# Performance work log

Measured on AMD Instinct MI355X. Metric: run time of the kernel, lower is better.

## Reference

```python
import jax, jax.numpy as jnp
import numpy as np

N_NODES = 100000


def _add_self_loops(edge_index, n):
    loop = jnp.arange(n, dtype=edge_index.dtype)
    src = jnp.concatenate([edge_index[0], loop])
    dst = jnp.concatenate([edge_index[1], loop])
    return src, dst


def _gcn_conv(x, W, b, src, dst, n):
    # h = X W, then symmetric-normalized scatter-add over edges (PyG GCNConv)
    h = x @ W
    ones = jnp.ones(src.shape[0], dtype=h.dtype)
    deg = jax.ops.segment_sum(ones, dst, num_segments=n)  # in-degree incl. self loops
    dinv = jnp.where(deg > 0, jax.lax.rsqrt(deg), 0.0)
    norm = dinv[src] * dinv[dst]                           # [E]
    msg = h[src] * norm[:, None]                           # gather + scale
    out = jax.ops.segment_sum(msg, dst, num_segments=n)    # scatter-add
    return out + b


def setup_inputs() -> dict:
    key = jax.random.key(0)
    k1, k2, k3, k4 = jax.random.split(key, 4)
    F, H, C = 128, 128, 16
    x = jax.random.normal(k1, (N_NODES, F), dtype=jnp.float32)
    edge_index = jax.random.randint(k2, (2, 1600000), 0, N_NODES, dtype=jnp.int64)
    W1 = jax.random.normal(k3, (F, H), dtype=jnp.float32) / np.sqrt(F)
    b1 = jnp.zeros((H,), dtype=jnp.float32)
    W2 = jax.random.normal(k4, (H, C), dtype=jnp.float32) / np.sqrt(H)
    b2 = jnp.zeros((C,), dtype=jnp.float32)
    return {"x": x, "edge_index": edge_index, "W1": W1, "b1": b1, "W2": W2, "b2": b2}


def reference(x, edge_index, W1, b1, W2, b2):
    n = x.shape[0]
    src, dst = _add_self_loops(edge_index, n)
    h = _gcn_conv(x, W1, b1, src, dst, n)
    h = jax.nn.relu(h)
    # dropout(p=0.1) treated as identity (deterministic eval-mode reference)
    logits = _gcn_conv(h, W2, b2, src, dst, n)
    return logits, jax.nn.log_softmax(logits, axis=1)
```

## Files before the change

### kernel.cpp

```cpp
#include <hip/hip_runtime.h>
#include <math.h>


#define ELLW 72
#define EPB 16384
#define BSH 9
#define MAXEB 100
#define MAXBK 200

typedef __attribute__((ext_vector_type(8))) short short8;
typedef __attribute__((ext_vector_type(4))) float f32x4;
typedef __attribute__((ext_vector_type(4))) int i32x4;
typedef __attribute__((ext_vector_type(4))) _Float16 f16x4;

__device__ __forceinline__ float bf2f(unsigned short u) {
    return __uint_as_float(((unsigned int)u) << 16);
}
__device__ __forceinline__ unsigned short f2bf(float f) {
    unsigned int u = __float_as_uint(f);
    unsigned int r = (u + 0x7fffu + ((u >> 16) & 1u)) >> 16;
    return (unsigned short)r;
}
__device__ __forceinline__ f32x4 h2f4(f16x4 v) {
    f32x4 r;
    r[0] = (float)v[0]; r[1] = (float)v[1]; r[2] = (float)v[2]; r[3] = (float)v[3];
    return r;
}

__global__ void k_prep_hist(unsigned short* __restrict__ h, _Float16* __restrict__ g,
                            const float* __restrict__ W1, unsigned short* __restrict__ wt,
                            int n, const int* __restrict__ dst, int E,
                            int* __restrict__ hist, int nbuck) {
    __shared__ int lh[MAXBK];
    const int t = threadIdx.x;
    if (blockIdx.x < 64) {
        int i = blockIdx.x * 256 + t;
        if (i < 16384) {
            int nc = i >> 7, k = i & 127;
            wt[i] = f2bf(W1[k * 128 + nc]);
        }
        if (i < 128) h[(size_t)n * 128 + i] = 0;
        if (i < 16) g[(size_t)n * 16 + i] = (_Float16)0.f;
        return;
    }
    const int blk = blockIdx.x - 64;
    for (int i = t; i < nbuck; i += 256) lh[i] = 0;
    __syncthreads();
    const int e0 = blk * EPB;
    const int e1 = min(e0 + EPB, E);
    for (int e = e0 + t; e < e1; e += 256)
        atomicAdd(&lh[dst[e] >> BSH], 1);
    __syncthreads();
    for (int i = t; i < nbuck; i += 256)
        hist[blk * nbuck + i] = lh[i];
}

__global__ void k_scan(int* __restrict__ hist, int* __restrict__ bstart,
                       int* __restrict__ bcount, int neb, int nbuck) {
    __shared__ unsigned short lh[MAXEB * MAXBK];
    __shared__ int sc[256];
    const int t = threadIdx.x;
    const int items = neb * nbuck;
    const int it4 = items >> 2;
    for (int i = t; i < it4; i += 256) {
        i32x4 v = *(const i32x4*)(hist + i * 4);
        lh[i * 4 + 0] = (unsigned short)v[0];
        lh[i * 4 + 1] = (unsigned short)v[1];
        lh[i * 4 + 2] = (unsigned short)v[2];
        lh[i * 4 + 3] = (unsigned short)v[3];
    }
    for (int i = (it4 << 2) + t; i < items; i += 256)
        lh[i] = (unsigned short)hist[i];
    __syncthreads();
    int total = 0;
    if (t < nbuck)
        for (int blk = 0; blk < neb; ++blk) total += lh[blk * nbuck + t];
    sc[t] = total;
    __syncthreads();
    for (int o = 1; o < 256; o <<= 1) {
        int x = 0;
        if (t >= o) x = sc[t - o];
        __syncthreads();
        if (t >= o) sc[t] += x;
        __syncthreads();
    }
    if (t < nbuck) {
        int run = sc[t] - total;
        bstart[t] = run;
        bcount[t] = total;
        for (int blk = 0; blk < neb; ++blk) {
            int idx = blk * nbuck + t;
            int v = lh[idx];
            hist[idx] = run;
            run += v;
        }
    }
}

__global__ void k_bin(const int* __restrict__ src, const int* __restrict__ dst, int E,
                      const int* __restrict__ hist, int* __restrict__ binned, int nbuck) {
    __shared__ int cnt[MAXBK];
    const int t = threadIdx.x, blk = blockIdx.x;
    for (int i = t; i < nbuck; i += 256) cnt[i] = hist[blk * nbuck + i];
    __syncthreads();
    const int e0 = blk * EPB;
    const int e1 = min(e0 + EPB, E);
    for (int e = e0 + t; e < e1; e += 256) {
        int d = dst[e];
        int b = d >> BSH;
        int pos = atomicAdd(&cnt[b], 1);
        binned[pos] = src[e] | ((d & ((1 << BSH) - 1)) << 17);
    }
}

__global__ void k_ell(const int* __restrict__ binned, const int* __restrict__ bstart,
                      const int* __restrict__ bcount, int* __restrict__ deg,
                      int* __restrict__ col, int n) {
    __shared__ int ldeg[1 << BSH];
    const int t = threadIdx.x, b = blockIdx.x;
    const int node0 = b << BSH;
    for (int i = t; i < (1 << BSH); i += 256) ldeg[i] = 0;
    __syncthreads();
    const int st = bstart[b], cv = bcount[b];
    for (int i = t; i < cv; i += 256) {
        int v = binned[st + i];
        int s = v & 0x1FFFF;
        int dl = v >> 17;
        int q = atomicAdd(&ldeg[dl], 1);
        if (q < ELLW) col[(size_t)(node0 + dl) * ELLW + q] = s;
    }
    __syncthreads();
    for (int i = t; i < (1 << BSH); i += 256) {
        int node = node0 + i;
        if (node < n) {
            int dgv = ldeg[i];
            deg[node] = dgv;
            int dc = dgv > ELLW ? ELLW : dgv;
            int kend = (dc + 7) & ~7;
            for (int q = dc; q < kend; ++q) col[(size_t)node * ELLW + q] = n;
        }
    }
}

__global__ void k_gemm1(const float* __restrict__ x, const unsigned short* __restrict__ wt,
                        const int* __restrict__ deg, unsigned short* __restrict__ h,
                        int n) {
    __shared__ unsigned short xs[64 * 136];
    const int t = threadIdx.x;
    const int row0 = blockIdx.x * 64;
    for (int i = t; i < 2048; i += 256) {
        int r = i >> 5, c4 = (i & 31) << 2;
        int gr = row0 + r;
        float4 v = make_float4(0.f, 0.f, 0.f, 0.f);
        if (gr < n) v = *(const float4*)(x + (size_t)gr * 128 + c4);
        ushort4 u;
        u.x = f2bf(v.x); u.y = f2bf(v.y); u.z = f2bf(v.z); u.w = f2bf(v.w);
        *(ushort4*)(xs + r * 136 + c4) = u;
    }
    __syncthreads();
    const int w = t >> 6;
    const int lane = t & 63;
    const int m = lane & 15, q = lane >> 4;
    f32x4 acc[8];
#pragma unroll
    for (int ns = 0; ns < 8; ++ns) acc[ns] = (f32x4){0.f, 0.f, 0.f, 0.f};
#pragma unroll
    for (int kt = 0; kt < 4; ++kt) {
        short8 a = *(const short8*)(xs + (w * 16 + m) * 136 + kt * 32 + q * 8);
#pragma unroll
        for (int ns = 0; ns < 8; ++ns) {
            short8 b = *(const short8*)((const short*)wt + (ns * 16 + m) * 128 + kt * 32 + q * 8);
            acc[ns] = __builtin_amdgcn_mfma_f32_16x16x32_bf16(a, b, acc[ns], 0, 0, 0);
        }
    }
    unsigned short* xsw = xs + (w * 16) * 136;
    float srow[4];
#pragma unroll
    for (int reg = 0; reg < 4; ++reg) {
        int gr = row0 + w * 16 + q * 4 + reg;
        srow[reg] = (gr < n) ? rsqrtf((float)(deg[gr] + 1)) : 0.f;
    }
#pragma unroll
    for (int ns = 0; ns < 8; ++ns)
#pragma unroll
        for (int reg = 0; reg < 4; ++reg)
            xsw[(q * 4 + reg) * 136 + ns * 16 + m] = f2bf(acc[ns][reg] * srow[reg]);
    __syncthreads();
#pragma unroll
    for (int it = 0; it < 8; ++it) {
        int rl = (lane >> 5) + it * 2;
        int off = (lane & 31) * 4;
        int gr = row0 + w * 16 + rl;
        if (gr < n)
            *(ushort4*)(h + (size_t)gr * 128 + off) = *(const ushort4*)(xsw + rl * 136 + off);
    }
}

__global__ __launch_bounds__(256, 2) void k_gather1f(
        const unsigned short* __restrict__ h, const int* __restrict__ deg,
        const int* __restrict__ col, const float* __restrict__ b1,
        const float* __restrict__ W2, _Float16* __restrict__ g, int n) {
    const int t = threadIdx.x;
    const int lane = t & 15;
    const int d = blockIdx.x * 16 + (t >> 4);
    if (d >= n) return;
    int dg = deg[d];
    if (dg > ELLW) dg = ELLW;
    const float dd = rsqrtf((float)(dg + 1));
    const int kend = (dg + 7) & ~7;
    const int* ecol = col + (size_t)d * ELLW;

    float aA[8], aB[8];
    {
        short8 u = *(const short8*)(h + (size_t)d * 128 + lane * 8);
#pragma unroll
        for (int j = 0; j < 8; ++j) {
            aA[j] = bf2f((unsigned short)u[j]);
            aB[j] = 0.f;
        }
    }
    for (int k = 0; k < kend; k += 8) {
        int4 c0 = *(const int4*)(ecol + k);
        int4 c1 = *(const int4*)(ecol + k + 4);
        short8 u0 = *(const short8*)(h + (size_t)c0.x * 128 + lane * 8);
        short8 u1 = *(const short8*)(h + (size_t)c0.y * 128 + lane * 8);
        short8 u2 = *(const short8*)(h + (size_t)c0.z * 128 + lane * 8);
        short8 u3 = *(const short8*)(h + (size_t)c0.w * 128 + lane * 8);
        short8 u4 = *(const short8*)(h + (size_t)c1.x * 128 + lane * 8);
        short8 u5 = *(const short8*)(h + (size_t)c1.y * 128 + lane * 8);
        short8 u6 = *(const short8*)(h + (size_t)c1.z * 128 + lane * 8);
        short8 u7 = *(const short8*)(h + (size_t)c1.w * 128 + lane * 8);
#pragma unroll
        for (int j = 0; j < 8; ++j) {
            aA[j] += bf2f((unsigned short)u0[j]) + bf2f((unsigned short)u2[j]) +
                     bf2f((unsigned short)u4[j]) + bf2f((unsigned short)u6[j]);
            aB[j] += bf2f((unsigned short)u1[j]) + bf2f((unsigned short)u3[j]) +
                     bf2f((unsigned short)u5[j]) + bf2f((unsigned short)u7[j]);
        }
    }
    float y[8];
    const float* b1p = b1 + lane * 8;
#pragma unroll
    for (int j = 0; j < 8; ++j)
        y[j] = fmaxf(fmaf(aA[j] + aB[j], dd, b1p[j]), 0.f);
    const float4* w2v = (const float4*)(W2 + lane * 8 * 16);
    float4 z0 = make_float4(0.f, 0.f, 0.f, 0.f);
    float4 z1 = z0, z2 = z0, z3 = z0;
#pragma unroll
    for (int j = 0; j < 8; ++j) {
        float4 w0 = w2v[j * 4 + 0], w1 = w2v[j * 4 + 1];
        float4 w2 = w2v[j * 4 + 2], w3 = w2v[j * 4 + 3];
        float yj = y[j];
        z0.x = fmaf(yj, w0.x, z0.x); z0.y = fmaf(yj, w0.y, z0.y);
        z0.z = fmaf(yj, w0.z, z0.z); z0.w = fmaf(yj, w0.w, z0.w);
        z1.x = fmaf(yj, w1.x, z1.x); z1.y = fmaf(yj, w1.y, z1.y);
        z1.z = fmaf(yj, w1.z, z1.z); z1.w = fmaf(yj, w1.w, z1.w);
        z2.x = fmaf(yj, w2.x, z2.x); z2.y = fmaf(yj, w2.y, z2.y);
        z2.z = fmaf(yj, w2.z, z2.z); z2.w = fmaf(yj, w2.w, z2.w);
        z3.x = fmaf(yj, w3.x, z3.x); z3.y = fmaf(yj, w3.y, z3.y);
        z3.z = fmaf(yj, w3.z, z3.z); z3.w = fmaf(yj, w3.w, z3.w);
    }
#pragma unroll
    for (int mm = 1; mm < 16; mm <<= 1) {
        z0.x += __shfl_xor(z0.x, mm); z0.y += __shfl_xor(z0.y, mm);
        z0.z += __shfl_xor(z0.z, mm); z0.w += __shfl_xor(z0.w, mm);
        z1.x += __shfl_xor(z1.x, mm); z1.y += __shfl_xor(z1.y, mm);
        z1.z += __shfl_xor(z1.z, mm); z1.w += __shfl_xor(z1.w, mm);
        z2.x += __shfl_xor(z2.x, mm); z2.y += __shfl_xor(z2.y, mm);
        z2.z += __shfl_xor(z2.z, mm); z2.w += __shfl_xor(z2.w, mm);
        z3.x += __shfl_xor(z3.x, mm); z3.y += __shfl_xor(z3.y, mm);
        z3.z += __shfl_xor(z3.z, mm); z3.w += __shfl_xor(z3.w, mm);
    }
    if (lane < 4) {
        float4 z = (lane == 0) ? z0 : (lane == 1) ? z1 : (lane == 2) ? z2 : z3;
        f16x4 zz;
        zz[0] = (_Float16)(z.x * dd); zz[1] = (_Float16)(z.y * dd);
        zz[2] = (_Float16)(z.z * dd); zz[3] = (_Float16)(z.w * dd);
        *(f16x4*)(g + (size_t)d * 16 + lane * 4) = zz;
    }
}

__global__ void k_gather2(const _Float16* __restrict__ g, const int* __restrict__ deg,
                          const int* __restrict__ col, const float* __restrict__ b2,
                          float* __restrict__ out, int n) {
    const int t = threadIdx.x;
    const int d = blockIdx.x * 64 + (t >> 2);
    if (d >= n) return;
    const int l = t & 3;
    int dg = deg[d];
    if (dg > ELLW) dg = ELLW;
    const float dd = rsqrtf((float)(dg + 1));
    const int kend = (dg + 7) & ~7;
    const int* ecol = col + (size_t)d * ELLW;
    const _Float16* gl = g + l * 4;

    f32x4 aA = h2f4(*(const f16x4*)(gl + (size_t)d * 16));
    f32x4 aB = (f32x4){0.f, 0.f, 0.f, 0.f};
    f32x4 aC = aB, aD = aB;
    for (int k = 0; k < kend; k += 8) {
        int4 c0 = *(const int4*)(ecol + k);
        int4 c1 = *(const int4*)(ecol + k + 4);
        f16x4 h0 = *(const f16x4*)(gl + (size_t)c0.x * 16);
        f16x4 h1 = *(const f16x4*)(gl + (size_t)c0.y * 16);
        f16x4 h2 = *(const f16x4*)(gl + (size_t)c0.z * 16);
        f16x4 h3 = *(const f16x4*)(gl + (size_t)c0.w * 16);
        f16x4 h4 = *(const f16x4*)(gl + (size_t)c1.x * 16);
        f16x4 h5 = *(const f16x4*)(gl + (size_t)c1.y * 16);
        f16x4 h6 = *(const f16x4*)(gl + (size_t)c1.z * 16);
        f16x4 h7 = *(const f16x4*)(gl + (size_t)c1.w * 16);
        aA += h2f4(h0); aB += h2f4(h1); aC += h2f4(h2); aD += h2f4(h3);
        aA += h2f4(h4); aB += h2f4(h5); aC += h2f4(h6); aD += h2f4(h7);
    }
    f32x4 bv = *(const f32x4*)(b2 + l * 4);
    f32x4 acc = (aA + aB + aC + aD) * dd + bv;
    *(f32x4*)(out + (size_t)d * 16 + l * 4) = acc;
    float m = fmaxf(fmaxf(acc[0], acc[1]), fmaxf(acc[2], acc[3]));
    m = fmaxf(m, __shfl_xor(m, 1));
    m = fmaxf(m, __shfl_xor(m, 2));
    float e = expf(acc[0] - m) + expf(acc[1] - m) + expf(acc[2] - m) + expf(acc[3] - m);
    e += __shfl_xor(e, 1);
    e += __shfl_xor(e, 2);
    float ls = m + logf(e);
    f32x4 o;
    o[0] = acc[0] - ls; o[1] = acc[1] - ls; o[2] = acc[2] - ls; o[3] = acc[3] - ls;
    *(f32x4*)(out + (size_t)n * 16 + (size_t)d * 16 + l * 4) = o;
}

static inline size_t align256(size_t v) { return (v + 255) & ~(size_t)255; }

extern "C" void kernel_launch(void* const* d_in, const int* in_sizes, int n_in,
                              void* d_out, int out_size, void* d_ws, size_t ws_size,
                              hipStream_t stream) {
    const float* x  = (const float*)d_in[0];
    const int*   ei = (const int*)d_in[1];
    const float* W1 = (const float*)d_in[2];
    const float* b1 = (const float*)d_in[3];
    const float* W2 = (const float*)d_in[4];
    const float* b2 = (const float*)d_in[5];
    float* out = (float*)d_out;

    const int n = in_sizes[0] / 128;
    const int E = in_sizes[1] / 2;
    const int* src = ei;
    const int* dst = ei + E;
    const int NEB = (E + EPB - 1) / EPB;
    const int NBUCK = (n + (1 << BSH) - 1) >> BSH;

    char* base = (char*)d_ws;
    size_t off = 0;
    int* deg = (int*)(base + off); off = align256(off + (size_t)n * 4);
    int* col = (int*)(base + off); off = align256(off + (size_t)n * ELLW * 4);
    unsigned short* wt = (unsigned short*)(base + off); off = align256(off + 128 * 128 * 2);
    unsigned short* h = (unsigned short*)(base + off); off = align256(off + ((size_t)n + 1) * 128 * 2);
    _Float16* g = (_Float16*)(base + off); off = align256(off + ((size_t)n + 1) * 16 * 2);
    int* hist = (int*)(base + off); off = align256(off + (size_t)MAXEB * MAXBK * 4);
    int* bstart = (int*)(base + off); off = align256(off + (size_t)MAXBK * 4);
    int* bcount = (int*)(base + off); off = align256(off + (size_t)MAXBK * 4);
    int* binned = (int*)(base + off); off = align256(off + (size_t)E * 4);

    k_prep_hist<<<64 + NEB, 256, 0, stream>>>(h, g, W1, wt, n, dst, E, hist, NBUCK);
    k_scan<<<1, 256, 0, stream>>>(hist, bstart, bcount, NEB, NBUCK);
    k_bin<<<NEB, 256, 0, stream>>>(src, dst, E, hist, binned, NBUCK);
    k_ell<<<NBUCK, 256, 0, stream>>>(binned, bstart, bcount, deg, col, n);

    k_gemm1<<<(n + 63) / 64, 256, 0, stream>>>(x, wt, deg, h, n);
    k_gather1f<<<(n + 15) / 16, 256, 0, stream>>>(h, deg, col, b1, W2, g, n);

    k_gather2<<<(n + 63) / 64, 256, 0, stream>>>(g, deg, col, b2, out, n);
}
```

Measured before the change: 351.4 us.

## Merge edge binning with GEMM1 and move degree normalization into gather

Binning blocks and GEMM1 blocks now run in one launch, so the dense XW1 product overlaps the edge binning and no longer has to wait for degrees. Because GEMM1 can run before degrees are known, the source-side scaling leaves the GEMM epilogue. A per-node dinv array is built in k_ell and applied per neighbour inside gather1f. This costs an extra 4-byte gather per edge, replaces adds with FMAs, and changes the rounding order, since h is now stored unscaled in bf16.

```diff
diff --git a/kernel.cpp b/kernel.cpp
--- a/kernel.cpp
+++ b/kernel.cpp
@@ -30,7 +30,7 @@
 __global__ void k_prep_hist(unsigned short* __restrict__ h, _Float16* __restrict__ g,
                             const float* __restrict__ W1, unsigned short* __restrict__ wt,
                             int n, const int* __restrict__ dst, int E,
-                            int* __restrict__ hist, int nbuck) {
+                            int* __restrict__ hist, int nbuck, float* __restrict__ dinv) {
     __shared__ int lh[MAXBK];
     const int t = threadIdx.x;
     if (blockIdx.x < 64) {
@@ -41,6 +41,7 @@
         }
         if (i < 128) h[(size_t)n * 128 + i] = 0;
         if (i < 16) g[(size_t)n * 16 + i] = (_Float16)0.f;
+        if (i < 1) dinv[n] = 1.f;
         return;
     }
     const int blk = blockIdx.x - 64;
@@ -97,57 +98,29 @@
     }
 }
 
-__global__ void k_bin(const int* __restrict__ src, const int* __restrict__ dst, int E,
-                      const int* __restrict__ hist, int* __restrict__ binned, int nbuck) {
-    __shared__ int cnt[MAXBK];
-    const int t = threadIdx.x, blk = blockIdx.x;
-    for (int i = t; i < nbuck; i += 256) cnt[i] = hist[blk * nbuck + i];
-    __syncthreads();
-    const int e0 = blk * EPB;
-    const int e1 = min(e0 + EPB, E);
-    for (int e = e0 + t; e < e1; e += 256) {
-        int d = dst[e];
-        int b = d >> BSH;
-        int pos = atomicAdd(&cnt[b], 1);
-        binned[pos] = src[e] | ((d & ((1 << BSH) - 1)) << 17);
-    }
-}
-
-__global__ void k_ell(const int* __restrict__ binned, const int* __restrict__ bstart,
-                      const int* __restrict__ bcount, int* __restrict__ deg,
-                      int* __restrict__ col, int n) {
-    __shared__ int ldeg[1 << BSH];
-    const int t = threadIdx.x, b = blockIdx.x;
-    const int node0 = b << BSH;
-    for (int i = t; i < (1 << BSH); i += 256) ldeg[i] = 0;
-    __syncthreads();
-    const int st = bstart[b], cv = bcount[b];
-    for (int i = t; i < cv; i += 256) {
-        int v = binned[st + i];
-        int s = v & 0x1FFFF;
-        int dl = v >> 17;
-        int q = atomicAdd(&ldeg[dl], 1);
-        if (q < ELLW) col[(size_t)(node0 + dl) * ELLW + q] = s;
-    }
-    __syncthreads();
-    for (int i = t; i < (1 << BSH); i += 256) {
-        int node = node0 + i;
-        if (node < n) {
-            int dgv = ldeg[i];
-            deg[node] = dgv;
-            int dc = dgv > ELLW ? ELLW : dgv;
-            int kend = (dc + 7) & ~7;
-            for (int q = dc; q < kend; ++q) col[(size_t)node * ELLW + q] = n;
-        }
-    }
-}
-
-__global__ void k_gemm1(const float* __restrict__ x, const unsigned short* __restrict__ wt,
-                        const int* __restrict__ deg, unsigned short* __restrict__ h,
-                        int n) {
+__global__ __launch_bounds__(256) void k_bin_gemm(
+        const int* __restrict__ src, const int* __restrict__ dst, int E,
+        const int* __restrict__ hist, int* __restrict__ binned, int nbuck, int neb,
+        const float* __restrict__ x, const unsigned short* __restrict__ wt,
+        unsigned short* __restrict__ h, int n) {
     __shared__ unsigned short xs[64 * 136];
     const int t = threadIdx.x;
-    const int row0 = blockIdx.x * 64;
+    if ((int)blockIdx.x < neb) {
+        int* cnt = (int*)xs;
+        const int blk = blockIdx.x;
+        for (int i = t; i < nbuck; i += 256) cnt[i] = hist[blk * nbuck + i];
+        __syncthreads();
+        const int e0 = blk * EPB;
+        const int e1 = min(e0 + EPB, E);
+        for (int e = e0 + t; e < e1; e += 256) {
+            int d = dst[e];
+            int b = d >> BSH;
+            int pos = atomicAdd(&cnt[b], 1);
+            binned[pos] = src[e] | ((d & ((1 << BSH) - 1)) << 17);
+        }
+        return;
+    }
+    const int row0 = ((int)blockIdx.x - neb) * 64;
     for (int i = t; i < 2048; i += 256) {
         int r = i >> 5, c4 = (i & 31) << 2;
         int gr = row0 + r;
@@ -174,17 +147,11 @@
         }
     }
     unsigned short* xsw = xs + (w * 16) * 136;
-    float srow[4];
-#pragma unroll
-    for (int reg = 0; reg < 4; ++reg) {
-        int gr = row0 + w * 16 + q * 4 + reg;
-        srow[reg] = (gr < n) ? rsqrtf((float)(deg[gr] + 1)) : 0.f;
-    }
 #pragma unroll
     for (int ns = 0; ns < 8; ++ns)
 #pragma unroll
         for (int reg = 0; reg < 4; ++reg)
-            xsw[(q * 4 + reg) * 136 + ns * 16 + m] = f2bf(acc[ns][reg] * srow[reg]);
+            xsw[(q * 4 + reg) * 136 + ns * 16 + m] = f2bf(acc[ns][reg]);
     __syncthreads();
 #pragma unroll
     for (int it = 0; it < 8; ++it) {
@@ -196,17 +163,48 @@
     }
 }
 
+__global__ void k_ell(const int* __restrict__ binned, const int* __restrict__ bstart,
+                      const int* __restrict__ bcount, int* __restrict__ deg,
+                      float* __restrict__ dinv, int* __restrict__ col, int n) {
+    __shared__ int ldeg[1 << BSH];
+    const int t = threadIdx.x, b = blockIdx.x;
+    const int node0 = b << BSH;
+    for (int i = t; i < (1 << BSH); i += 256) ldeg[i] = 0;
+    __syncthreads();
+    const int st = bstart[b], cv = bcount[b];
+    for (int i = t; i < cv; i += 256) {
+        int v = binned[st + i];
+        int s = v & 0x1FFFF;
+        int dl = v >> 17;
+        int q = atomicAdd(&ldeg[dl], 1);
+        if (q < ELLW) col[(size_t)(node0 + dl) * ELLW + q] = s;
+    }
+    __syncthreads();
+    for (int i = t; i < (1 << BSH); i += 256) {
+        int node = node0 + i;
+        if (node < n) {
+            int dgv = ldeg[i];
+            deg[node] = dgv;
+            int dc = dgv > ELLW ? ELLW : dgv;
+            dinv[node] = rsqrtf((float)(dc + 1));
+            int kend = (dc + 7) & ~7;
+            for (int q = dc; q < kend; ++q) col[(size_t)node * ELLW + q] = n;
+        }
+    }
+}
+
 __global__ __launch_bounds__(256, 2) void k_gather1f(
         const unsigned short* __restrict__ h, const int* __restrict__ deg,
-        const int* __restrict__ col, const float* __restrict__ b1,
-        const float* __restrict__ W2, _Float16* __restrict__ g, int n) {
+        const float* __restrict__ dinv, const int* __restrict__ col,
+        const float* __restrict__ b1, const float* __restrict__ W2,
+        _Float16* __restrict__ g, int n) {
     const int t = threadIdx.x;
     const int lane = t & 15;
     const int d = blockIdx.x * 16 + (t >> 4);
     if (d >= n) return;
     int dg = deg[d];
     if (dg > ELLW) dg = ELLW;
-    const float dd = rsqrtf((float)(dg + 1));
+    const float dd = dinv[d];
     const int kend = (dg + 7) & ~7;
     const int* ecol = col + (size_t)d * ELLW;
 
@@ -215,13 +213,15 @@
         short8 u = *(const short8*)(h + (size_t)d * 128 + lane * 8);
 #pragma unroll
         for (int j = 0; j < 8; ++j) {
-            aA[j] = bf2f((unsigned short)u[j]);
+            aA[j] = dd * bf2f((unsigned short)u[j]);
             aB[j] = 0.f;
         }
     }
     for (int k = 0; k < kend; k += 8) {
         int4 c0 = *(const int4*)(ecol + k);
         int4 c1 = *(const int4*)(ecol + k + 4);
+        float e0 = dinv[c0.x], e1 = dinv[c0.y], e2 = dinv[c0.z], e3 = dinv[c0.w];
+        float e4 = dinv[c1.x], e5 = dinv[c1.y], e6 = dinv[c1.z], e7 = dinv[c1.w];
         short8 u0 = *(const short8*)(h + (size_t)c0.x * 128 + lane * 8);
         short8 u1 = *(const short8*)(h + (size_t)c0.y * 128 + lane * 8);
         short8 u2 = *(const short8*)(h + (size_t)c0.z * 128 + lane * 8);
@@ -232,10 +232,14 @@
         short8 u7 = *(const short8*)(h + (size_t)c1.w * 128 + lane * 8);
 #pragma unroll
         for (int j = 0; j < 8; ++j) {
-            aA[j] += bf2f((unsigned short)u0[j]) + bf2f((unsigned short)u2[j]) +
-                     bf2f((unsigned short)u4[j]) + bf2f((unsigned short)u6[j]);
-            aB[j] += bf2f((unsigned short)u1[j]) + bf2f((unsigned short)u3[j]) +
-                     bf2f((unsigned short)u5[j]) + bf2f((unsigned short)u7[j]);
+            aA[j] = fmaf(bf2f((unsigned short)u0[j]), e0, aA[j]);
+            aB[j] = fmaf(bf2f((unsigned short)u1[j]), e1, aB[j]);
+            aA[j] = fmaf(bf2f((unsigned short)u2[j]), e2, aA[j]);
+            aB[j] = fmaf(bf2f((unsigned short)u3[j]), e3, aB[j]);
+            aA[j] = fmaf(bf2f((unsigned short)u4[j]), e4, aA[j]);
+            aB[j] = fmaf(bf2f((unsigned short)u5[j]), e5, aB[j]);
+            aA[j] = fmaf(bf2f((unsigned short)u6[j]), e6, aA[j]);
+            aB[j] = fmaf(bf2f((unsigned short)u7[j]), e7, aB[j]);
         }
     }
     float y[8];
@@ -349,6 +353,7 @@
     char* base = (char*)d_ws;
     size_t off = 0;
     int* deg = (int*)(base + off); off = align256(off + (size_t)n * 4);
+    float* dinv = (float*)(base + off); off = align256(off + ((size_t)n + 1) * 4);
     int* col = (int*)(base + off); off = align256(off + (size_t)n * ELLW * 4);
     unsigned short* wt = (unsigned short*)(base + off); off = align256(off + 128 * 128 * 2);
     unsigned short* h = (unsigned short*)(base + off); off = align256(off + ((size_t)n + 1) * 128 * 2);
@@ -358,13 +363,13 @@
     int* bcount = (int*)(base + off); off = align256(off + (size_t)MAXBK * 4);
     int* binned = (int*)(base + off); off = align256(off + (size_t)E * 4);
 
-    k_prep_hist<<<64 + NEB, 256, 0, stream>>>(h, g, W1, wt, n, dst, E, hist, NBUCK);
+    k_prep_hist<<<64 + NEB, 256, 0, stream>>>(h, g, W1, wt, n, dst, E, hist, NBUCK, dinv);
     k_scan<<<1, 256, 0, stream>>>(hist, bstart, bcount, NEB, NBUCK);
-    k_bin<<<NEB, 256, 0, stream>>>(src, dst, E, hist, binned, NBUCK);
-    k_ell<<<NBUCK, 256, 0, stream>>>(binned, bstart, bcount, deg, col, n);
-
-    k_gemm1<<<(n + 63) / 64, 256, 0, stream>>>(x, wt, deg, h, n);
-    k_gather1f<<<(n + 15) / 16, 256, 0, stream>>>(h, deg, col, b1, W2, g, n);
+    k_bin_gemm<<<NEB + (n + 63) / 64, 256, 0, stream>>>(
+        src, dst, E, hist, binned, NBUCK, NEB, x, wt, h, n);
+    k_ell<<<NBUCK, 256, 0, stream>>>(binned, bstart, bcount, deg, dinv, col, n);
+
+    k_gather1f<<<(n + 15) / 16, 256, 0, stream>>>(h, deg, dinv, col, b1, W2, g, n);
 
     k_gather2<<<(n + 63) / 64, 256, 0, stream>>>(g, deg, col, b2, out, n);
 }
```

Result: no change. 347.7 us (-1.1%).
